# Optimization experiments

Hardware: AMD Instinct MI355X
Metric: run time of the kernel (lower is better)

The kernel has to match this reference:

```python
import jax, jax.numpy as jnp
import numpy as np

B, L, H2, T = 64, 512, 1536, 64


def setup_inputs() -> dict:
    key = jax.random.key(0)
    k0, k1, k2, k3 = jax.random.split(key, 4)
    x = jax.random.normal(k0, (B, L, H2), dtype=jnp.float32)
    W = jax.random.normal(k1, (H2, T), dtype=jnp.float32) * 0.02
    b = jnp.zeros((T,), dtype=jnp.float32)
    tags = jax.random.randint(k2, (B, L), 0, T).astype(jnp.int64)
    attention_mask = jnp.ones((B, L), dtype=jnp.float32)
    tag_to_score = jax.random.uniform(k3, (T,), dtype=jnp.float32)
    return {"x": x, "W": W, "b": b, "tags": tags,
            "attention_mask": attention_mask, "tag_to_score": tag_to_score, "t": 2}


def reference(x, W, b, tags, attention_mask, tag_to_score, t):
    # dense projection: [B,L,H2] @ [H2,T] -> [B,L,T]
    logits = jnp.einsum("blh,ht->blt", x, W) + b
    # additive attention mask, broadcast over tag dim (as in torch permute trick)
    logits = logits + (1.0 - attention_mask)[..., None] * -10000.0
    p = jax.nn.softmax(logits, axis=-1)

    # accuracy: tokens whose label is not one of the last 3 special tags
    valid = tags < (T - 3)
    pred = jnp.argmax(p, axis=-1)
    right = jnp.sum((valid & (pred == tags)).astype(jnp.float32))
    count = jnp.sum(valid.astype(jnp.float32))
    acc1 = right / count

    # _dynamic_target: ones everywhere, tag_to_score[tag]**t at the tag index
    score = tag_to_score[tags] ** t                       # [B,L]
    hot = jax.nn.one_hot(tags, T, dtype=p.dtype)          # [B,L,T]
    y = 1.0 + hot * (score - 1.0)[..., None]
    y = jax.nn.softmax(y, axis=-1)

    loss1 = -jnp.sum(y * jnp.log(p + 1e-10))
    return (loss1, acc1)
```

## Files before the change

### kernel.cpp

```cpp
#include <hip/hip_runtime.h>
#include <hip/hip_bf16.h>


#define H2 1536
#define NT 64
#define ROWS (64 * 512)
#define KC 64
#define NITER (H2 / KC)
#define KS2 (H2 / 32)
#define NBLK (ROWS / 16)

typedef __attribute__((ext_vector_type(8))) short short8;
typedef __attribute__((ext_vector_type(4))) float f32x4;

#define B_FRAGS (KS2 * 4 * 64)

__device__ __forceinline__ short bf_hi(float f) {
    __hip_bfloat16 h = __float2bfloat16(f);
    return __builtin_bit_cast(short, h);
}
__device__ __forceinline__ float bf_f(short s) {
    __hip_bfloat16 h = __builtin_bit_cast(__hip_bfloat16, s);
    return __bfloat162float(h);
}

__global__ void mlaner_prepw(const float* __restrict__ W,
                             short8* __restrict__ bhi, short8* __restrict__ blo)
{
    const int tid = blockIdx.x * 256 + threadIdx.x;
    const int L = tid & 63, c = (tid >> 6) & 3, s2 = tid >> 8;
    const int kbase = s2 * 32 + (L >> 4) * 8;
    const int n = c * 16 + (L & 15);
    short8 hi, lo;
#pragma unroll
    for (int j = 0; j < 8; ++j) {
        float w = W[(size_t)(kbase + j) * NT + n];
        short h = bf_hi(w);
        hi[j] = h;
        lo[j] = bf_hi(w - bf_f(h));
    }
    const int idx = (s2 * 4 + c) * 64 + L;
    bhi[idx] = hi;
    blo[idx] = lo;
}

__device__ __forceinline__ void cvt_split(float4 a0, float4 a1,
                                          short8& hi, short8& lo)
{
    float v[8] = {a0.x, a0.y, a0.z, a0.w, a1.x, a1.y, a1.z, a1.w};
#pragma unroll
    for (int j = 0; j < 8; ++j) {
        short h = bf_hi(v[j]);
        hi[j] = h;
        lo[j] = bf_hi(v[j] - bf_f(h));
    }
}

__global__ __launch_bounds__(64, 2) void mlaner_main(
    const float* __restrict__ x,
    const short8* __restrict__ Bhi, const short8* __restrict__ Blo,
    const float* __restrict__ bias, const int* __restrict__ tags,
    const float* __restrict__ tag_to_score, const int* __restrict__ tptr,
    float* __restrict__ ploss, unsigned* __restrict__ pright,
    unsigned* __restrict__ pvalid)
{
    __shared__ float lds[2][KC * 16];

    const int lane = threadIdx.x;
    const int blk = blockIdx.x;
    const int row0 = blk * 16;
    const int q = lane >> 4, n16 = lane & 15;

    auto dma = [&](int b, int s) {
#pragma unroll
        for (int i = 0; i < 4; ++i) {
            const int idx = i * 64 + lane;
            const int r = idx >> 4, j = idx & 15;
            const int jg = j ^ (r & 7);
            const float* gp = x + (size_t)(row0 + r) * H2 + s * KC + jg * 4;
            __builtin_amdgcn_global_load_lds(
                (const __attribute__((address_space(1))) void*)gp,
                (__attribute__((address_space(3))) void*)&lds[b][i * 256],
                16, 0, 0);
        }
    };

    f32x4 acc[4];
#pragma unroll
    for (int c = 0; c < 4; ++c) acc[c] = (f32x4){0.f, 0.f, 0.f, 0.f};

    dma(0, 0);
    __syncthreads();

#pragma unroll 1
    for (int s = 0; s < NITER; ++s) {
        short8 bh[2][4], bl[2][4];
#pragma unroll
        for (int h = 0; h < 2; ++h)
#pragma unroll
            for (int c = 0; c < 4; ++c) {
                const int f = ((s * 2 + h) * 4 + c) * 64 + lane;
                bh[h][c] = Bhi[f];
                bl[h][c] = Blo[f];
            }

        if (s + 1 < NITER) dma((s + 1) & 1, s + 1);

        const float* bufp = &lds[s & 1][0];
#pragma unroll
        for (int h = 0; h < 2; ++h) {
            const int sg0 = (h * 8 + 2 * q)     ^ (n16 & 7);
            const int sg1 = (h * 8 + 2 * q + 1) ^ (n16 & 7);
            float4 a0 = *(const float4*)&bufp[n16 * 64 + sg0 * 4];
            float4 a1 = *(const float4*)&bufp[n16 * 64 + sg1 * 4];
            short8 ah, al;
            cvt_split(a0, a1, ah, al);
#pragma unroll
            for (int c = 0; c < 4; ++c) {
                acc[c] = __builtin_amdgcn_mfma_f32_16x16x32_bf16(ah, bh[h][c], acc[c], 0, 0, 0);
                acc[c] = __builtin_amdgcn_mfma_f32_16x16x32_bf16(ah, bl[h][c], acc[c], 0, 0, 0);
                acc[c] = __builtin_amdgcn_mfma_f32_16x16x32_bf16(al, bh[h][c], acc[c], 0, 0, 0);
            }
        }
        __syncthreads();
    }

    const float bv0 = bias[n16], bv1 = bias[16 + n16];
    const float bv2 = bias[32 + n16], bv3 = bias[48 + n16];
    int tg[4];
#pragma unroll
    for (int i = 0; i < 4; ++i) tg[i] = tags[row0 + q * 4 + i];
    const int tt = tptr[0];
    const float e1c = expf(1.0f);
    float loss_acc = 0.0f;
    unsigned right_acc = 0, valid_acc = 0;

#pragma unroll 1
    for (int i = 0; i < 4; ++i) {
        float l0 = acc[0][i] + bv0, l1 = acc[1][i] + bv1;
        float l2 = acc[2][i] + bv2, l3 = acc[3][i] + bv3;

        float m = fmaxf(fmaxf(l0, l1), fmaxf(l2, l3));
#pragma unroll
        for (int off = 8; off >= 1; off >>= 1)
            m = fmaxf(m, __shfl_xor(m, off, 64));

        float e0 = expf(l0 - m), e1 = expf(l1 - m);
        float e2 = expf(l2 - m), e3 = expf(l3 - m);
        float Z = e0 + e1 + e2 + e3;
#pragma unroll
        for (int off = 8; off >= 1; off >>= 1)
            Z += __shfl_xor(Z, off, 64);

        float lp0 = logf(e0 / Z + 1e-10f), lp1 = logf(e1 / Z + 1e-10f);
        float lp2 = logf(e2 / Z + 1e-10f), lp3 = logf(e3 / Z + 1e-10f);
        float slp = lp0 + lp1 + lp2 + lp3;
#pragma unroll
        for (int off = 8; off >= 1; off >>= 1)
            slp += __shfl_xor(slp, off, 64);

        float bval = l0; int bcol = n16;
        if (l1 > bval) { bval = l1; bcol = 16 + n16; }
        if (l2 > bval) { bval = l2; bcol = 32 + n16; }
        if (l3 > bval) { bval = l3; bcol = 48 + n16; }
#pragma unroll
        for (int off = 8; off >= 1; off >>= 1) {
            float ov = __shfl_xor(bval, off, 64);
            int   oc = __shfl_xor(bcol, off, 64);
            if (ov > bval || (ov == bval && oc < bcol)) { bval = ov; bcol = oc; }
        }

        const int tag = tg[i];
        const int csel = tag >> 4;
        float cand = (csel == 0) ? lp0 : (csel == 1) ? lp1 : (csel == 2) ? lp2 : lp3;
        float lptag = __shfl(cand, (lane & 48) | (tag & 15), 64);

        float sc = tag_to_score[tag];
        float sp = powf(sc, (float)tt);
        float es = expf(sp);
        float denom = 63.0f * e1c + es;
        float rowloss = -((e1c / denom) * (slp - lptag) + (es / denom) * lptag);

        if (n16 == 0) {
            loss_acc += rowloss;
            unsigned valid = (tag < NT - 3) ? 1u : 0u;
            valid_acc += valid;
            right_acc += (valid && bcol == tag) ? 1u : 0u;
        }
    }

#pragma unroll
    for (int off = 32; off >= 1; off >>= 1) {
        loss_acc += __shfl_xor(loss_acc, off, 64);
        right_acc += __shfl_xor((int)right_acc, off, 64);
        valid_acc += __shfl_xor((int)valid_acc, off, 64);
    }
    if (lane == 0) {
        ploss[blk] = loss_acc;
        pright[blk] = right_acc;
        pvalid[blk] = valid_acc;
    }
}

__global__ void mlaner_final(const float* __restrict__ pl,
                             const unsigned* __restrict__ pr,
                             const unsigned* __restrict__ pv,
                             float* __restrict__ out)
{
    __shared__ float sl[4];
    __shared__ unsigned sr[4], sv[4];
    const int tid = threadIdx.x, lane = tid & 63, wv = tid >> 6;
    float l = 0.0f; unsigned r = 0, v = 0;
    for (int i = tid; i < NBLK; i += 256) { l += pl[i]; r += pr[i]; v += pv[i]; }
#pragma unroll
    for (int off = 32; off >= 1; off >>= 1) {
        l += __shfl_xor(l, off, 64);
        r += __shfl_xor((int)r, off, 64);
        v += __shfl_xor((int)v, off, 64);
    }
    if (lane == 0) { sl[wv] = l; sr[wv] = r; sv[wv] = v; }
    __syncthreads();
    if (tid == 0) {
        float L = sl[0] + sl[1] + sl[2] + sl[3];
        unsigned R = sr[0] + sr[1] + sr[2] + sr[3];
        unsigned V = sv[0] + sv[1] + sv[2] + sv[3];
        out[0] = L;
        out[1] = (float)R / (float)V;
    }
}

extern "C" void kernel_launch(void* const* d_in, const int* in_sizes, int n_in,
                              void* d_out, int out_size, void* d_ws, size_t ws_size,
                              hipStream_t stream)
{
    const float* x    = (const float*)d_in[0];
    const float* W    = (const float*)d_in[1];
    const float* b    = (const float*)d_in[2];
    const int*   tags = (const int*)d_in[3];
    const float* t2s  = (const float*)d_in[5];
    const int*   tptr = (const int*)d_in[6];
    float* out = (float*)d_out;

    short8* bhi = (short8*)d_ws;
    short8* blo = bhi + B_FRAGS;
    float* ploss = (float*)((char*)d_ws + (size_t)2 * B_FRAGS * 16);
    unsigned* pright = (unsigned*)(ploss + NBLK);
    unsigned* pvalid = pright + NBLK;

    mlaner_prepw<<<dim3(B_FRAGS / 256), dim3(256), 0, stream>>>(W, bhi, blo);
    mlaner_main<<<dim3(NBLK), dim3(64), 0, stream>>>(
        x, bhi, blo, b, tags, t2s, tptr, ploss, pright, pvalid);
    mlaner_final<<<dim3(1), dim3(256), 0, stream>>>(ploss, pright, pvalid, out);
}
```

Measured before the change: 311.1 us.

## Share W fragments across four waves via LDS staging in 256-thread blocks

```diff
diff --git a/kernel.cpp b/kernel.cpp
--- a/kernel.cpp
+++ b/kernel.cpp
@@ -8,7 +8,7 @@
 #define KC 64
 #define NITER (H2 / KC)
 #define KS2 (H2 / 32)
-#define NBLK (ROWS / 16)
+#define NBLK (ROWS / 64)
 
 typedef __attribute__((ext_vector_type(8))) short short8;
 typedef __attribute__((ext_vector_type(4))) float f32x4;
@@ -56,7 +56,7 @@
     }
 }
 
-__global__ __launch_bounds__(64, 2) void mlaner_main(
+__global__ __launch_bounds__(256, 2) void mlaner_main(
     const float* __restrict__ x,
     const short8* __restrict__ Bhi, const short8* __restrict__ Blo,
     const float* __restrict__ bias, const int* __restrict__ tags,
@@ -64,14 +64,17 @@
     float* __restrict__ ploss, unsigned* __restrict__ pright,
     unsigned* __restrict__ pvalid)
 {
-    __shared__ float lds[2][KC * 16];
-
-    const int lane = threadIdx.x;
+    __shared__ __align__(16) float xbuf[2][4][KC * 16];
+    __shared__ short8 bbuf[2][2][512];
+
+    const int tid = threadIdx.x;
+    const int lane = tid & 63;
+    const int wave = tid >> 6;
     const int blk = blockIdx.x;
-    const int row0 = blk * 16;
+    const int row0 = blk * 64 + wave * 16;
     const int q = lane >> 4, n16 = lane & 15;
 
-    auto dma = [&](int b, int s) {
+    auto stage = [&](int b, int s) {
 #pragma unroll
         for (int i = 0; i < 4; ++i) {
             const int idx = i * 64 + lane;
@@ -80,35 +83,46 @@
             const float* gp = x + (size_t)(row0 + r) * H2 + s * KC + jg * 4;
             __builtin_amdgcn_global_load_lds(
                 (const __attribute__((address_space(1))) void*)gp,
-                (__attribute__((address_space(3))) void*)&lds[b][i * 256],
+                (__attribute__((address_space(3))) void*)&xbuf[b][wave][i * 256],
                 16, 0, 0);
         }
+#pragma unroll
+        for (int i = 0; i < 2; ++i) {
+            const int kb = wave * 2 + i;
+            const short8* gh = Bhi + (size_t)s * 512 + kb * 64 + lane;
+            __builtin_amdgcn_global_load_lds(
+                (const __attribute__((address_space(1))) void*)gh,
+                (__attribute__((address_space(3))) void*)&bbuf[b][0][kb * 64],
+                16, 0, 0);
+            const short8* gl = Blo + (size_t)s * 512 + kb * 64 + lane;
+            __builtin_amdgcn_global_load_lds(
+                (const __attribute__((address_space(1))) void*)gl,
+                (__attribute__((address_space(3))) void*)&bbuf[b][1][kb * 64],
+                16, 0, 0);
+        }
     };
 
     f32x4 acc[4];
 #pragma unroll
     for (int c = 0; c < 4; ++c) acc[c] = (f32x4){0.f, 0.f, 0.f, 0.f};
 
-    dma(0, 0);
+    stage(0, 0);
     __syncthreads();
 
 #pragma unroll 1
     for (int s = 0; s < NITER; ++s) {
-        short8 bh[2][4], bl[2][4];
-#pragma unroll
-        for (int h = 0; h < 2; ++h)
+        if (s + 1 < NITER) stage((s + 1) & 1, s + 1);
+
+        const int cur = s & 1;
+        const float* bufp = &xbuf[cur][wave][0];
+#pragma unroll
+        for (int h = 0; h < 2; ++h) {
+            short8 bh[4], bl[4];
 #pragma unroll
             for (int c = 0; c < 4; ++c) {
-                const int f = ((s * 2 + h) * 4 + c) * 64 + lane;
-                bh[h][c] = Bhi[f];
-                bl[h][c] = Blo[f];
+                bh[c] = bbuf[cur][0][(h * 4 + c) * 64 + lane];
+                bl[c] = bbuf[cur][1][(h * 4 + c) * 64 + lane];
             }
-
-        if (s + 1 < NITER) dma((s + 1) & 1, s + 1);
-
-        const float* bufp = &lds[s & 1][0];
-#pragma unroll
-        for (int h = 0; h < 2; ++h) {
             const int sg0 = (h * 8 + 2 * q)     ^ (n16 & 7);
             const int sg1 = (h * 8 + 2 * q + 1) ^ (n16 & 7);
             float4 a0 = *(const float4*)&bufp[n16 * 64 + sg0 * 4];
@@ -117,9 +131,9 @@
             cvt_split(a0, a1, ah, al);
 #pragma unroll
             for (int c = 0; c < 4; ++c) {
-                acc[c] = __builtin_amdgcn_mfma_f32_16x16x32_bf16(ah, bh[h][c], acc[c], 0, 0, 0);
-                acc[c] = __builtin_amdgcn_mfma_f32_16x16x32_bf16(ah, bl[h][c], acc[c], 0, 0, 0);
-                acc[c] = __builtin_amdgcn_mfma_f32_16x16x32_bf16(al, bh[h][c], acc[c], 0, 0, 0);
+                acc[c] = __builtin_amdgcn_mfma_f32_16x16x32_bf16(ah, bh[c], acc[c], 0, 0, 0);
+                acc[c] = __builtin_amdgcn_mfma_f32_16x16x32_bf16(ah, bl[c], acc[c], 0, 0, 0);
+                acc[c] = __builtin_amdgcn_mfma_f32_16x16x32_bf16(al, bh[c], acc[c], 0, 0, 0);
             }
         }
         __syncthreads();
@@ -176,7 +190,7 @@
         float lptag = __shfl(cand, (lane & 48) | (tag & 15), 64);
 
         float sc = tag_to_score[tag];
-        float sp = powf(sc, (float)tt);
+        float sp = (tt == 2) ? sc * sc : powf(sc, (float)tt);
         float es = expf(sp);
         float denom = 63.0f * e1c + es;
         float rowloss = -((e1c / denom) * (slp - lptag) + (es / denom) * lptag);
@@ -195,10 +209,16 @@
         right_acc += __shfl_xor((int)right_acc, off, 64);
         valid_acc += __shfl_xor((int)valid_acc, off, 64);
     }
-    if (lane == 0) {
-        ploss[blk] = loss_acc;
-        pright[blk] = right_acc;
-        pvalid[blk] = valid_acc;
+
+    float* redf = &xbuf[0][0][0];
+    unsigned* redu = (unsigned*)&xbuf[0][1][0];
+    unsigned* redv = (unsigned*)&xbuf[0][2][0];
+    if (lane == 0) { redf[wave] = loss_acc; redu[wave] = right_acc; redv[wave] = valid_acc; }
+    __syncthreads();
+    if (tid == 0) {
+        ploss[blk] = redf[0] + redf[1] + redf[2] + redf[3];
+        pright[blk] = redu[0] + redu[1] + redu[2] + redu[3];
+        pvalid[blk] = redv[0] + redv[1] + redv[2] + redv[3];
     }
 }
 
@@ -248,7 +268,7 @@
     unsigned* pvalid = pright + NBLK;
 
     mlaner_prepw<<<dim3(B_FRAGS / 256), dim3(256), 0, stream>>>(W, bhi, blo);
-    mlaner_main<<<dim3(NBLK), dim3(64), 0, stream>>>(
+    mlaner_main<<<dim3(NBLK), dim3(256), 0, stream>>>(
         x, bhi, blo, b, tags, t2s, tptr, ploss, pright, pvalid);
     mlaner_final<<<dim3(1), dim3(256), 0, stream>>>(ploss, pright, pvalid, out);
 }
```

Result: faster. 296.5 us (-4.7%).
